# Kernel optimization log

Measured on AMD Instinct MI355X. Metric: run time of the kernel, lower is better.

The kernel has to match this reference:

```python
import jax, jax.numpy as jnp
import numpy as np

IMG = 64
NZ = 100
ENC_H = 800
DEC_H = 1600
IN_SZ = IMG * IMG  # 4096
D_ENC_IN = 2 * IN_SZ * 3 + DEC_H  # 26176


def setup_inputs() -> dict:
    key = jax.random.key(0)
    ks = jax.random.split(key, 12)
    B, T = 64, 10
    s = 0.02  # weight init scale to keep gates in sane range
    return {
        "x": jax.random.uniform(ks[0], (B, 3, IMG, IMG), jnp.float32),
        "noise": jax.random.normal(ks[1], (T, B, NZ), jnp.float32),
        "W_ih_mu": jax.random.normal(ks[2], (4 * ENC_H, D_ENC_IN), jnp.float32) * s,
        "W_hh_mu": jax.random.normal(ks[3], (4 * ENC_H, ENC_H), jnp.float32) * s,
        "b_mu": jnp.zeros((4 * ENC_H,), jnp.float32),
        "W_ih_lv": jax.random.normal(ks[4], (4 * ENC_H, D_ENC_IN), jnp.float32) * s,
        "W_hh_lv": jax.random.normal(ks[5], (4 * ENC_H, ENC_H), jnp.float32) * s,
        "b_lv": jnp.zeros((4 * ENC_H,), jnp.float32),
        "W_mu_fc": jax.random.normal(ks[6], (NZ, ENC_H), jnp.float32) * s,
        "b_mu_fc": jnp.zeros((NZ,), jnp.float32),
        "W_lv_fc": jax.random.normal(ks[7], (NZ, ENC_H), jnp.float32) * s,
        "b_lv_fc": jnp.zeros((NZ,), jnp.float32),
        "W_ih_dec": jax.random.normal(ks[8], (4 * DEC_H, NZ), jnp.float32) * s,
        "W_hh_dec": jax.random.normal(ks[9], (4 * DEC_H, DEC_H), jnp.float32) * s,
        "b_dec": jnp.zeros((4 * DEC_H,), jnp.float32),
        "W_write": jax.random.normal(ks[10], (3 * IN_SZ, DEC_H), jnp.float32) * s,
        "b_write": jnp.zeros((3 * IN_SZ,), jnp.float32),
        "T": T,
    }


def _lstm_cell(xin, h, c, W_ih, W_hh, b):
    # torch LSTMCell: gates ordered i, f, g, o
    g = xin @ W_ih.T + h @ W_hh.T + b
    i, f, gg, o = jnp.split(g, 4, axis=1)
    c_new = jax.nn.sigmoid(f) * c + jax.nn.sigmoid(i) * jnp.tanh(gg)
    h_new = jax.nn.sigmoid(o) * jnp.tanh(c_new)
    return h_new, c_new


def reference(x, noise, W_ih_mu, W_hh_mu, b_mu, W_ih_lv, W_hh_lv, b_lv,
              W_mu_fc, b_mu_fc, W_lv_fc, b_lv_fc,
              W_ih_dec, W_hh_dec, b_dec, W_write, b_write, T):
    B = x.shape[0]
    x_flat = x.reshape(B, -1)  # [B, 3*64*64]
    init = (
        jnp.zeros((B, 3, IMG, IMG), x.dtype),   # canvas c
        jnp.zeros((B, ENC_H), x.dtype), jnp.zeros((B, ENC_H), x.dtype),  # h_mu, c_mu
        jnp.zeros((B, ENC_H), x.dtype), jnp.zeros((B, ENC_H), x.dtype),  # h_lv, c_lv
        jnp.zeros((B, DEC_H), x.dtype), jnp.zeros((B, DEC_H), x.dtype),  # h_dec, c_dec
    )

    def step(carry, eps):
        c, h_mu, c_mu, h_lv, c_lv, h_dec, c_dec = carry
        sb = jax.nn.sigmoid(c)
        x_hat = (x - sb).reshape(B, -1)
        enc_in = jnp.concatenate([x_flat, x_hat, h_dec], axis=1)  # [B, 26176]
        h_mu, c_mu = _lstm_cell(enc_in, h_mu, c_mu, W_ih_mu, W_hh_mu, b_mu)
        mu = jax.nn.relu(h_mu @ W_mu_fc.T + b_mu_fc)
        h_lv, c_lv = _lstm_cell(enc_in, h_lv, c_lv, W_ih_lv, W_hh_lv, b_lv)
        logvar = jax.nn.relu(h_lv @ W_lv_fc.T + b_lv_fc)
        z = eps * jnp.exp(0.5 * logvar) + mu
        h_dec, c_dec = _lstm_cell(z, h_dec, c_dec, W_ih_dec, W_hh_dec, b_dec)
        wr = (h_dec @ W_write.T + b_write).reshape(B, 3, IMG, IMG)
        c = c + wr
        return (c, h_mu, c_mu, h_lv, c_lv, h_dec, c_dec), (mu, logvar)

    (c, *_), (mu_t, logvar_t) = jax.lax.scan(step, init, noise)
    return jax.nn.sigmoid(c), mu_t, logvar_t
```

## Files before the change

kernel.cpp:

```cpp
#include <hip/hip_runtime.h>

typedef __attribute__((ext_vector_type(8))) short bf16x8;
typedef __attribute__((ext_vector_type(4))) float f32x4;
typedef __attribute__((ext_vector_type(4))) int i32x4;
typedef unsigned int u32;

#define B_SZ   64
#define IMGSZ  12288
#define ENC_H  800
#define DEC_H  1600
#define NZ     100
#define NENC   6400
#define KHH    832
#define KDEC   1728
#define GSZ    (B_SZ*NENC)
#define SLICES 7
#define G0SL   8

#define WQMUL    1008.0f
#define SCALE_I8 (-1.0f/(254.0f*1008.0f))

__device__ __forceinline__ unsigned short f2bf(float f){
  unsigned u = __float_as_uint(f);
  u += 0x7fffu + ((u >> 16) & 1u);
  return (unsigned short)(u >> 16);
}
__device__ __forceinline__ float bf2f(unsigned short h){
  return __uint_as_float(((unsigned)h) << 16);
}
__device__ __forceinline__ float sigf(float x){ return 1.f/(1.f + __expf(-x)); }
__device__ __forceinline__ ushort4 cv4(float4 v){
  ushort4 o; o.x=f2bf(v.x); o.y=f2bf(v.y); o.z=f2bf(v.z); o.w=f2bf(v.w); return o;
}
__device__ __forceinline__ unsigned q4(float4 v){
  int a = __float2int_rn(fminf(fmaxf(v.x*WQMUL, -127.f), 127.f));
  int b = __float2int_rn(fminf(fmaxf(v.y*WQMUL, -127.f), 127.f));
  int c = __float2int_rn(fminf(fmaxf(v.z*WQMUL, -127.f), 127.f));
  int d = __float2int_rn(fminf(fmaxf(v.w*WQMUL, -127.f), 127.f));
  return (a&255) | ((b&255)<<8) | ((c&255)<<16) | ((d&255)<<24);
}

__device__ __forceinline__ void gllb(const void* g, void* l){
  __builtin_amdgcn_global_load_lds((const __attribute__((address_space(1))) u32*)g,
                                   (__attribute__((address_space(3))) u32*)l, 16, 0, 0);
}

__device__ __forceinline__ void gemm_lds3(const unsigned short* __restrict__ A, int lda, int k0,
                                          const unsigned short* __restrict__ Bpk, size_t bchunk0,
                                          int nchb, unsigned short (*sm)[4096], f32x4 acc[4])
{
  const int tid = threadIdx.x;
  const int lane = tid & 63, w = tid >> 6;
  const int l15 = lane & 15, lg = lane >> 4;
  const int l8 = lane >> 3, l7 = lane & 7;

  const unsigned short* gA0 = A + (size_t)(w*16 + l8)*lda + k0 + (l7 ^ l8)*8;
  const unsigned short* gA1 = gA0 + (size_t)8*lda;
  const unsigned short* gB0 = Bpk + bchunk0*4096 + w*1024 + lane*8;

#pragma unroll
  for (int m = 0; m < 4; ++m) acc[m] = (f32x4){0.f,0.f,0.f,0.f};

  gllb(gA0, &sm[0][(w*2+0)*512]);
  gllb(gA1, &sm[0][(w*2+1)*512]);
  gllb(gB0,       &sm[1][w*1024]);
  gllb(gB0 + 512, &sm[1][w*1024 + 512]);
  if (1 < nchb){
    gllb(gA0 + 64, &sm[2][(w*2+0)*512]);
    gllb(gA1 + 64, &sm[2][(w*2+1)*512]);
    gllb(gB0 + 4096,       &sm[3][w*1024]);
    gllb(gB0 + 4096 + 512, &sm[3][w*1024 + 512]);
  }

  int cur = 0, nxt = 2;
  for (int c = 0; c < nchb; ++c){
    if (c + 1 < nchb) { asm volatile("s_waitcnt vmcnt(4)" ::: "memory"); }
    else              { asm volatile("s_waitcnt vmcnt(0)" ::: "memory"); }
    asm volatile("s_barrier" ::: "memory");
    const unsigned short* sa = sm[cur*2];
    const unsigned short* sb = sm[cur*2 + 1];
#pragma unroll
    for (int h = 0; h < 2; ++h){
      const int su8 = ((h*4 + lg) ^ (l15 & 7)) * 8;
      bf16x8 bfr = *(const bf16x8*)&sb[(w*16 + l15)*64 + su8];
#pragma unroll
      for (int m = 0; m < 4; ++m){
        bf16x8 afr = *(const bf16x8*)&sa[(m*16 + l15)*64 + su8];
        acc[m] = __builtin_amdgcn_mfma_f32_16x16x32_bf16(afr, bfr, acc[m], 0,0,0);
      }
    }
    if (c + 2 < nchb){
      const size_t ao = (size_t)(c+2)*64, bo = (size_t)(c+2)*4096;
      gllb(gA0 + ao, &sm[nxt*2][(w*2+0)*512]);
      gllb(gA1 + ao, &sm[nxt*2][(w*2+1)*512]);
      gllb(gB0 + bo,       &sm[nxt*2+1][w*1024]);
      gllb(gB0 + bo + 512, &sm[nxt*2+1][w*1024 + 512]);
    }
    cur = (cur==2) ? 0 : cur+1;
    nxt = (nxt==2) ? 0 : nxt+1;
  }
}

__device__ __forceinline__ void gemm_i8(const signed char* __restrict__ A, int lda, int k0,
                                        const signed char* __restrict__ Bpk, size_t bch0,
                                        int nch, unsigned char* sm, i32x4 acc[4])
{
  const int tid = threadIdx.x;
  const int lane = tid & 63, w = tid >> 6;
  const int l15 = lane & 15, lg = lane >> 4;

  const int rp = lane >> 3, un = lane & 7;
  const int swz = un ^ (rp & 7);
  const int rloc = rp*2 + ((swz >> 2) & 1);
  const int uA = swz & 3;
  const signed char* gA = A + (size_t)(w*16 + rloc)*lda + k0 + uA*16;
  const signed char* gB = Bpk + bch0*4096 + w*1024 + lane*16;

#pragma unroll
  for (int m = 0; m < 4; ++m) acc[m] = (i32x4){0,0,0,0};

  {
    gllb(gA, sm + 0*8192 + w*1024 + lane*16);
    gllb(gB, sm + 0*8192 + 4096 + w*1024 + lane*16);
    if (1 < nch){
      gllb(gA + 64,   sm + 1*8192 + w*1024 + lane*16);
      gllb(gB + 4096, sm + 1*8192 + 4096 + w*1024 + lane*16);
    }
  }

  const int rB = w*16 + l15;
  const int offB = 4096 + (rB>>1)*128 + (((((rB&1)<<2) + lg) ^ ((rB>>1)&7))*16);

  int cur = 0, nxt = 2;
  for (int c = 0; c < nch; ++c){
    if (c + 1 < nch) { asm volatile("s_waitcnt vmcnt(2)" ::: "memory"); }
    else             { asm volatile("s_waitcnt vmcnt(0)" ::: "memory"); }
    asm volatile("s_barrier" ::: "memory");
    const unsigned char* s = sm + cur*8192;
    i32x4 bfr = *(const i32x4*)(s + offB);
#pragma unroll
    for (int m = 0; m < 4; ++m){
      int rA = m*16 + l15;
      i32x4 afr = *(const i32x4*)(s + (rA>>1)*128 + (((((rA&1)<<2) + lg) ^ ((rA>>1)&7))*16));
      acc[m] = __builtin_amdgcn_mfma_i32_16x16x64_i8(afr, bfr, acc[m], 0, 0, 0);
    }
    if (c + 2 < nch){
      gllb(gA + (size_t)(c+2)*64,   sm + nxt*8192 + w*1024 + lane*16);
      gllb(gB + (size_t)(c+2)*4096, sm + nxt*8192 + 4096 + w*1024 + lane*16);
    }
    cur = (cur==2) ? 0 : cur+1;
    nxt = (nxt==2) ? 0 : nxt+1;
  }
}

__device__ __forceinline__ void store_out1(f32x4 acc[4], float* __restrict__ Out,
                                           int ldo, int col0){
  const int lane = threadIdx.x & 63, w = threadIdx.x >> 6;
  const int l15 = lane & 15, lg = lane >> 4;
  int col = col0 + w*16 + l15;
#pragma unroll
  for (int m = 0; m < 4; ++m)
#pragma unroll
    for (int j = 0; j < 4; ++j)
      Out[(size_t)(m*16 + lg*4 + j)*ldo + col] = acc[m][j];
}

__device__ __forceinline__ void store_i8(i32x4 acc[4], float* __restrict__ Out,
                                         int ldo, int col0){
  const int lane = threadIdx.x & 63, w = threadIdx.x >> 6;
  const int l15 = lane & 15, lg = lane >> 4;
  int col = col0 + w*16 + l15;
#pragma unroll
  for (int m = 0; m < 4; ++m)
#pragma unroll
    for (int j = 0; j < 4; ++j)
      Out[(size_t)(m*16 + lg*4 + j)*ldo + col] = SCALE_I8 * (float)acc[m][j];
}

#define R_ENCM 19200
#define R_WHC  21700
#define R_WHH  23000
#define R_WDEC 25700
#define R_WWR  30500
#define R_MISC 31425
#define M_FC   40000u
#define M_XBF  236608u

__global__ __launch_bounds__(256) void k_pack_all(
    const float* __restrict__ Wihmu, const float* __restrict__ Wihlv,
    const float* __restrict__ Whhmu, const float* __restrict__ Whhlv,
    const float* __restrict__ Whhdec, const float* __restrict__ Wihdec,
    const float* __restrict__ Wwrite, const float* __restrict__ Wmufc,
    const float* __restrict__ Wlvfc, const float* __restrict__ x,
    unsigned short* __restrict__ wab, unsigned char* __restrict__ wi8,
    float* __restrict__ csPart, unsigned short* __restrict__ whc,
    unsigned short* __restrict__ whh, unsigned short* __restrict__ wdec,
    unsigned short* __restrict__ wwr, unsigned short* __restrict__ wfcmu,
    unsigned short* __restrict__ wfclv, unsigned short* __restrict__ xbf)
{
  int bid = blockIdx.x;
  if (bid < R_ENCM){
    __shared__ float cs[256];
    int ch = bid % 192, cb = bid / 192;
    int t = threadIdx.x;
    int r = t >> 2, seg = t & 3;
    int col = cb*64 + r;
    const float4* src = (col < 3200) ? ((const float4*)Wihmu + (size_t)col*6544)
                                     : ((const float4*)Wihlv + (size_t)(col-3200)*6544);
    int k4b = ch*16 + seg*4;
    float4 va[4], vb[4];
#pragma unroll
    for (int i = 0; i < 4; ++i){ va[i] = src[k4b+i]; vb[i] = src[3072 + k4b + i]; }

    ushort4* wabT = (ushort4*)wab + ((size_t)cb*192 + ch)*1024;
#pragma unroll
    for (int d = 0; d < 2; ++d){
      int u16 = seg*2 + d;
      int su = u16 ^ (r & 7);
      float4 s0, s1;
      s0.x=va[2*d].x+vb[2*d].x;   s0.y=va[2*d].y+vb[2*d].y;
      s0.z=va[2*d].z+vb[2*d].z;   s0.w=va[2*d].w+vb[2*d].w;
      s1.x=va[2*d+1].x+vb[2*d+1].x; s1.y=va[2*d+1].y+vb[2*d+1].y;
      s1.z=va[2*d+1].z+vb[2*d+1].z; s1.w=va[2*d+1].w+vb[2*d+1].w;
      wabT[r*16 + su*2 + 0] = cv4(s0);
      wabT[r*16 + su*2 + 1] = cv4(s1);
    }

    unsigned char* wi8T = wi8 + ((size_t)cb*192 + ch)*4096;
    int unit = (((r&1)<<2) + seg) ^ ((r>>1) & 7);
    uint4 pk;
    pk.x = q4(vb[0]); pk.y = q4(vb[1]); pk.z = q4(vb[2]); pk.w = q4(vb[3]);
    *(uint4*)(wi8T + (r>>1)*128 + unit*16) = pk;

    float s = 0.f;
#pragma unroll
    for (int i = 0; i < 4; ++i) s += vb[i].x + vb[i].y + vb[i].z + vb[i].w;
    cs[t] = s;
    __syncthreads();
    if (seg == 0)
      csPart[((size_t)col)*192 + ch] = cs[t] + cs[t+1] + cs[t+2] + cs[t+3];
  }
  else if (bid < R_WHC){
    int i = bid - R_ENCM;
    int ch = i % 25, cb = i / 25;
    ushort4* whcT = (ushort4*)whc + ((size_t)cb*25 + ch)*1024;
#pragma unroll
    for (int qv = 0; qv < 4; ++qv){
      int ou = qv*256 + threadIdx.x;
      int r = ou >> 4, qq = ou & 15;
      int su = qq >> 1, half = qq & 1;
      int uu = su ^ (r & 7);
      int k4 = ch*16 + uu*2 + half;
      int col = cb*64 + r;
      const float4* src = (col < 3200) ? ((const float4*)Wihmu + (size_t)col*6544)
                                       : ((const float4*)Wihlv + (size_t)(col-3200)*6544);
      whcT[ou] = cv4(src[6144 + k4]);
    }
  }
  else if (bid < R_WHH){
    int i = bid - R_WHC;
    int ch = i % 13, cb = i / 13;
    ushort4* whhT = (ushort4*)whh + ((size_t)cb*13 + ch)*1024;
#pragma unroll
    for (int qv = 0; qv < 4; ++qv){
      int ou = qv*256 + threadIdx.x;
      int r = ou >> 4, qq = ou & 15;
      int su = qq >> 1, half = qq & 1;
      int uu = su ^ (r & 7);
      int k4 = ch*16 + uu*2 + half;
      int col = cb*64 + r;
      float4 v = {0.f,0.f,0.f,0.f};
      if (k4 < 200)
        v = (col < 3200) ? ((const float4*)Whhmu)[(size_t)col*200 + k4]
                         : ((const float4*)Whhlv)[(size_t)(col-3200)*200 + k4];
      whhT[ou] = cv4(v);
    }
  }
  else if (bid < R_WDEC){
    int i = bid - R_WHH;
    int ch = i % 27, cb = i / 27;
    ushort4* wdecT = (ushort4*)wdec + ((size_t)cb*27 + ch)*1024;
#pragma unroll
    for (int qv = 0; qv < 4; ++qv){
      int ou = qv*256 + threadIdx.x;
      int r = ou >> 4, qq = ou & 15;
      int su = qq >> 1, half = qq & 1;
      int uu = su ^ (r & 7);
      int k4 = ch*16 + uu*2 + half;
      int pr = cb*64 + r;
      unsigned j = pr >> 2, g = pr & 3, srow = g*1600u + j;
      float4 v = {0.f,0.f,0.f,0.f};
      if (k4 < 400)      v = ((const float4*)Whhdec)[(size_t)srow*400 + k4];
      else if (k4 < 425) v = ((const float4*)Wihdec)[(size_t)srow*25 + (k4-400)];
      wdecT[ou] = cv4(v);
    }
  }
  else if (bid < R_WWR){
    int i = bid - R_WDEC;
    int ch = i % 25, cb = i / 25;
    ushort4* wwrT = (ushort4*)wwr + ((size_t)cb*25 + ch)*1024;
#pragma unroll
    for (int qv = 0; qv < 4; ++qv){
      int ou = qv*256 + threadIdx.x;
      int r = ou >> 4, qq = ou & 15;
      int su = qq >> 1, half = qq & 1;
      int uu = su ^ (r & 7);
      int k4 = ch*16 + uu*2 + half;
      int p = cb*64 + r;
      wwrT[ou] = cv4(((const float4*)Wwrite)[(size_t)p*400 + k4]);
    }
  }
  else {
    unsigned i = (unsigned)(bid - R_WWR)*256u + threadIdx.x;
    if (i >= M_XBF) return;
    if (i < M_FC){
      if (i < 20000u) ((ushort4*)wfcmu)[i] = cv4(((const float4*)Wmufc)[i]);
      else            ((ushort4*)wfclv)[i-20000u] = cv4(((const float4*)Wlvfc)[i-20000u]);
    } else {
      unsigned j = i - M_FC;
      ((ushort4*)xbf)[j] = cv4(((const float4*)x)[j]);
    }
  }
}

__global__ __launch_bounds__(256) void k_csred(const float* __restrict__ csPart,
                                               float* __restrict__ colsum){
  unsigned col = blockIdx.x*blockDim.x + threadIdx.x;
  if (col >= NENC) return;
  const float* p = csPart + (size_t)col*192;
  float s = 0.f;
#pragma unroll 8
  for (int ch = 0; ch < 192; ++ch) s += p[ch];
  colsum[col] = s;
}


__global__ __launch_bounds__(256) void k_g0(const unsigned short* __restrict__ xbf,
                                            const unsigned short* __restrict__ wab,
                                            float* __restrict__ gpart){
  __shared__ __align__(16) unsigned short smem[6][4096];
  int bid = blockIdx.x;
  int s = bid/100, cb = bid - s*100;
  f32x4 acc[4];
  gemm_lds3(xbf, IMGSZ, s*1536, wab, (size_t)cb*192 + s*24, 24, smem, acc);
  store_out1(acc, gpart + (size_t)s*GSZ, NENC, cb*64);
}

__global__ __launch_bounds__(256) void k_g0red(const float* __restrict__ gpart,
                                               float* __restrict__ g0){
  unsigned i = blockIdx.x*blockDim.x + threadIdx.x;
  if (i >= GSZ) return;
  float s = 0.f;
#pragma unroll
  for (int p = 0; p < G0SL; ++p) s += gpart[(size_t)p*GSZ + i];
  g0[i] = s;
}

__global__ __launch_bounds__(256) void k_enc(const signed char* __restrict__ ui8,
                                             const signed char* __restrict__ wi8,
                                             const unsigned short* __restrict__ uhd,
                                             const unsigned short* __restrict__ whc,
                                             const unsigned short* __restrict__ hmup,
                                             const unsigned short* __restrict__ hlvp,
                                             const unsigned short* __restrict__ whh,
                                             float* __restrict__ gpart){
  __shared__ __align__(16) unsigned char smem[49152];
  int bid = blockIdx.x;
  if (bid < 500){
    int s = bid/100, cb = bid - s*100;
    int ch0 = s*38 + (s < 2 ? s : 2);
    int nch = 38 + (s < 2 ? 1 : 0);
    i32x4 acc[4];
    gemm_i8(ui8, IMGSZ, ch0*64, wi8, (size_t)cb*192 + ch0, nch, smem, acc);
    store_i8(acc, gpart + (size_t)s*GSZ, NENC, cb*64);
  } else if (bid < 600){
    int cb = bid - 500;
    f32x4 acc[4];
    gemm_lds3(uhd, DEC_H, 0, whc, (size_t)cb*25, 25,
              (unsigned short (*)[4096])smem, acc);
    store_out1(acc, gpart + (size_t)5*GSZ, NENC, cb*64);
  } else {
    int cb = bid - 600;
    const unsigned short* A = (cb < 50) ? hmup : hlvp;
    f32x4 acc[4];
    gemm_lds3(A, KHH, 0, whh, (size_t)cb*13, 13,
              (unsigned short (*)[4096])smem, acc);
    store_out1(acc, gpart + (size_t)6*GSZ, NENC, cb*64);
  }
}

__global__ __launch_bounds__(512) void k_cell(const float* __restrict__ g0,
                                              const float* __restrict__ gpart,
                                              const float* __restrict__ colsum,
                                              const float* __restrict__ bmu,
                                              const float* __restrict__ blv,
                                              float* __restrict__ cmu,
                                              float* __restrict__ clv,
                                              unsigned short* __restrict__ hmup,
                                              unsigned short* __restrict__ hlvp,
                                              const unsigned short* __restrict__ wfcmu,
                                              const unsigned short* __restrict__ wfclv,
                                              const float* __restrict__ bmufc,
                                              const float* __restrict__ blvfc,
                                              const float* __restrict__ noise_t,
                                              float* __restrict__ outMu,
                                              float* __restrict__ outLv,
                                              unsigned short* __restrict__ u2z){
  __shared__ float hsh[1600];
  __shared__ float red[512];
  int b = blockIdx.x, tid = threadIdx.x;

  for (int uidx = tid; uidx < 1600; uidx += 512){
    int which = uidx >= 800;
    int j = uidx - which*800;
    const float* bias = which ? blv : bmu;
    int cbase = which*3200 + j;
    size_t rowoff = (size_t)b*NENC + cbase;
    float a0 = bias[j]       - 0.5f*colsum[cbase];
    float a1 = bias[800+j]   - 0.5f*colsum[cbase+800];
    float a2 = bias[1600+j]  - 0.5f*colsum[cbase+1600];
    float a3 = bias[2400+j]  - 0.5f*colsum[cbase+2400];
    const float* q = g0 + rowoff;
    a0 += q[0]; a1 += q[800]; a2 += q[1600]; a3 += q[2400];
#pragma unroll
    for (int s = 0; s < SLICES; ++s){
      const float* p = gpart + (size_t)s*GSZ + rowoff;
      a0 += p[0]; a1 += p[800]; a2 += p[1600]; a3 += p[2400];
    }
    float* C = which ? clv : cmu;
    float cold = C[(size_t)b*ENC_H + j];
    float cn = sigf(a1)*cold + sigf(a0)*tanhf(a2);
    float h  = sigf(a3)*tanhf(cn);
    C[(size_t)b*ENC_H + j] = cn;
    (which ? hlvp : hmup)[(size_t)b*KHH + j] = f2bf(h);
    hsh[uidx] = h;
  }
  __syncthreads();

  if (tid < 400){
    int o = tid >> 1, half = tid & 1;
    int ismu = o < 100;
    int row = ismu ? o : o - 100;
    const unsigned short* wrow = (ismu ? wfcmu : wfclv) + (size_t)row*ENC_H + half*400;
    const float* hbase = hsh + (ismu ? 0 : 800) + half*400;
    float s = 0.f;
#pragma unroll 4
    for (int k = 0; k < 100; ++k){
      ushort4 wv = ((const ushort4*)wrow)[k];
      s += bf2f(wv.x)*hbase[k*4]   + bf2f(wv.y)*hbase[k*4+1]
         + bf2f(wv.z)*hbase[k*4+2] + bf2f(wv.w)*hbase[k*4+3];
    }
    red[tid] = s;
  }
  __syncthreads();
  if (tid < 200){
    int o = tid; int ismu = o < 100; int row = ismu ? o : o - 100;
    float s = red[2*o] + red[2*o+1] + (ismu ? bmufc[row] : blvfc[row]);
    s = fmaxf(s, 0.f);
    if (ismu) outMu[(size_t)b*NZ + row] = s;
    else      outLv[(size_t)b*NZ + row] = s;
    hsh[o] = s;
  }
  __syncthreads();
  if (tid < 100){
    float mu = hsh[tid], lv = hsh[100 + tid];
    float z = noise_t[(size_t)b*NZ + tid]*__expf(0.5f*lv) + mu;
    u2z[(size_t)b*KDEC + DEC_H + tid] = f2bf(z);
  }
}

__global__ __launch_bounds__(256) void k_dec(const unsigned short* __restrict__ u2r,
                                             const unsigned short* __restrict__ wdec,
                                             const float* __restrict__ bdec,
                                             float* __restrict__ cdec,
                                             unsigned short* __restrict__ uhd,
                                             unsigned short* __restrict__ u2w){
  __shared__ __align__(16) unsigned short smem[6][4096];
  int bid = blockIdx.x;
  f32x4 acc[4];
  gemm_lds3(u2r, KDEC, 0, wdec, (size_t)bid*27, 27, smem, acc);
  __syncthreads();
  float* lds = (float*)&smem[0][0];
  const int lane = threadIdx.x & 63;
  const int wave = threadIdx.x >> 6;
  const int l15 = lane & 15, lg = lane >> 4;
#pragma unroll
  for (int m = 0; m < 4; ++m)
#pragma unroll
    for (int j = 0; j < 4; ++j)
      lds[(m*16 + lg*4 + j)*65 + wave*16 + l15] = acc[m][j];
  __syncthreads();
#pragma unroll
  for (int p = 0; p < 4; ++p){
    int idx = threadIdx.x + p*256;
    int b = idx & 63, jj = idx >> 6;
    const float* g4 = &lds[b*65 + jj*4];
    int j = bid*16 + jj;
    float gi = g4[0] + bdec[j];
    float gf = g4[1] + bdec[DEC_H + j];
    float gg = g4[2] + bdec[2*DEC_H + j];
    float go = g4[3] + bdec[3*DEC_H + j];
    float cold = cdec[(size_t)b*DEC_H + j];
    float cn = sigf(gf)*cold + sigf(gi)*tanhf(gg);
    float h  = sigf(go)*tanhf(cn);
    cdec[(size_t)b*DEC_H + j] = cn;
    unsigned short hb = f2bf(h);
    u2w[(size_t)b*KDEC + j] = hb;
    uhd[(size_t)b*DEC_H + j] = hb;
  }
}

__global__ __launch_bounds__(256) void k_write(const unsigned short* __restrict__ u2,
                                               const unsigned short* __restrict__ wwr,
                                               const float* __restrict__ bwr,
                                               float* __restrict__ canvas,
                                               signed char* __restrict__ ui8){
  __shared__ __align__(16) unsigned short smem[6][4096];
  f32x4 acc[4];
  gemm_lds3(u2, KDEC, 0, wwr, (size_t)blockIdx.x*25, 25, smem, acc);
  const int lane = threadIdx.x & 63;
  const int wave = threadIdx.x >> 6;
  const int l15 = lane & 15, lg = lane >> 4;
  int col = blockIdx.x*64 + wave*16 + l15;
#pragma unroll
  for (int m = 0; m < 4; ++m){
#pragma unroll
    for (int j = 0; j < 4; ++j){
      int row = m*16 + lg*4 + j;
      float cv = canvas[(size_t)row*IMGSZ + col] + acc[m][j] + bwr[col];
      canvas[(size_t)row*IMGSZ + col] = cv;
      ui8[(size_t)row*IMGSZ + col] =
        (signed char)__float2int_rn((sigf(cv) - 0.5f)*254.f);
    }
  }
}

__global__ __launch_bounds__(256) void k_final(const float* __restrict__ canvas,
                                               float* __restrict__ out){
  unsigned i = blockIdx.x*blockDim.x + threadIdx.x;
  if (i < (unsigned)(B_SZ*IMGSZ)) out[i] = sigf(canvas[i]);
}

constexpr size_t SZ_WAB    = (size_t)NENC*IMGSZ*2;
constexpr size_t SZ_WI8    = (size_t)NENC*IMGSZ;
constexpr size_t SZ_WHC    = (size_t)NENC*DEC_H*2;
constexpr size_t SZ_WHH    = (size_t)NENC*KHH*2;
constexpr size_t SZ_WDEC   = (size_t)NENC*KDEC*2;
constexpr size_t SZ_WWR    = (size_t)IMGSZ*DEC_H*2;
constexpr size_t SZ_WFC    = (size_t)NZ*ENC_H*2;
constexpr size_t SZ_XBF    = (size_t)B_SZ*IMGSZ*2;
constexpr size_t SZ_CSPART = (size_t)NENC*192*4;
constexpr size_t SZ_CSUM   = (size_t)NENC*4;
constexpr size_t SZ_G0     = (size_t)GSZ*4;
constexpr size_t SZ_GPART  = (size_t)G0SL*GSZ*4;
constexpr size_t SZ_CANVAS = (size_t)B_SZ*IMGSZ*4;
constexpr size_t SZ_CMU    = (size_t)B_SZ*ENC_H*4;
constexpr size_t SZ_CDEC   = (size_t)B_SZ*DEC_H*4;
constexpr size_t SZ_HP     = (size_t)B_SZ*KHH*2;
constexpr size_t SZ_UHD    = (size_t)B_SZ*DEC_H*2;
constexpr size_t SZ_U2     = (size_t)B_SZ*KDEC*2;
constexpr size_t SZ_UI8    = (size_t)B_SZ*IMGSZ;

constexpr size_t OFF_WAB    = 0;
constexpr size_t OFF_WI8    = OFF_WAB    + SZ_WAB;
constexpr size_t OFF_WHC    = OFF_WI8    + SZ_WI8;
constexpr size_t OFF_WHH    = OFF_WHC    + SZ_WHC;
constexpr size_t OFF_WDEC   = OFF_WHH    + SZ_WHH;
constexpr size_t OFF_WWR    = OFF_WDEC   + SZ_WDEC;
constexpr size_t OFF_WFCMU  = OFF_WWR    + SZ_WWR;
constexpr size_t OFF_WFCLV  = OFF_WFCMU  + SZ_WFC;
constexpr size_t OFF_XBF    = OFF_WFCLV  + SZ_WFC;
constexpr size_t OFF_CSPART = OFF_XBF    + SZ_XBF;
constexpr size_t OFF_CSUM   = OFF_CSPART + SZ_CSPART;
constexpr size_t OFF_G0     = OFF_CSUM   + SZ_CSUM;
constexpr size_t OFF_GPART  = OFF_G0     + SZ_G0;
constexpr size_t OFF_CANVAS = OFF_GPART  + SZ_GPART;
constexpr size_t OFF_CMU    = OFF_CANVAS + SZ_CANVAS;
constexpr size_t OFF_CLV    = OFF_CMU    + SZ_CMU;
constexpr size_t OFF_CDEC   = OFF_CLV    + SZ_CMU;
constexpr size_t OFF_HMUP   = OFF_CDEC   + SZ_CDEC;
constexpr size_t OFF_HLVP   = OFF_HMUP   + SZ_HP;
constexpr size_t OFF_UHD    = OFF_HLVP   + SZ_HP;
constexpr size_t OFF_U2A    = OFF_UHD    + SZ_UHD;
constexpr size_t OFF_U2B    = OFF_U2A    + SZ_U2;
constexpr size_t OFF_UI8    = OFF_U2B    + SZ_U2;
constexpr size_t OFF_END    = OFF_UI8    + SZ_UI8;

extern "C" void kernel_launch(void* const* d_in, const int* in_sizes, int n_in,
                              void* d_out, int out_size, void* d_ws, size_t ws_size,
                              hipStream_t stream) {
  const float* x      = (const float*)d_in[0];
  const float* noise  = (const float*)d_in[1];
  const float* Wihmu  = (const float*)d_in[2];
  const float* Whhmu  = (const float*)d_in[3];
  const float* bmu    = (const float*)d_in[4];
  const float* Wihlv  = (const float*)d_in[5];
  const float* Whhlv  = (const float*)d_in[6];
  const float* blv    = (const float*)d_in[7];
  const float* Wmufc  = (const float*)d_in[8];
  const float* bmufc  = (const float*)d_in[9];
  const float* Wlvfc  = (const float*)d_in[10];
  const float* blvfc  = (const float*)d_in[11];
  const float* Wihdec = (const float*)d_in[12];
  const float* Whhdec = (const float*)d_in[13];
  const float* bdec   = (const float*)d_in[14];
  const float* Wwrite = (const float*)d_in[15];
  const float* bwrite = (const float*)d_in[16];
  int T = in_sizes[1] / (B_SZ*NZ);

  if (ws_size < OFF_END) return;

  char* ws = (char*)d_ws;
  unsigned short* wab   = (unsigned short*)(ws + OFF_WAB);
  unsigned char*  wi8   = (unsigned char*)(ws + OFF_WI8);
  unsigned short* whc   = (unsigned short*)(ws + OFF_WHC);
  unsigned short* whh   = (unsigned short*)(ws + OFF_WHH);
  unsigned short* wdec  = (unsigned short*)(ws + OFF_WDEC);
  unsigned short* wwr   = (unsigned short*)(ws + OFF_WWR);
  unsigned short* wfcmu = (unsigned short*)(ws + OFF_WFCMU);
  unsigned short* wfclv = (unsigned short*)(ws + OFF_WFCLV);
  unsigned short* xbf   = (unsigned short*)(ws + OFF_XBF);
  float* csPart = (float*)(ws + OFF_CSPART);
  float* colsum = (float*)(ws + OFF_CSUM);
  float* g0     = (float*)(ws + OFF_G0);
  float* gpart  = (float*)(ws + OFF_GPART);
  float* canvas = (float*)(ws + OFF_CANVAS);
  float* cmu    = (float*)(ws + OFF_CMU);
  float* clv    = (float*)(ws + OFF_CLV);
  float* cdec   = (float*)(ws + OFF_CDEC);
  unsigned short* hmup = (unsigned short*)(ws + OFF_HMUP);
  unsigned short* hlvp = (unsigned short*)(ws + OFF_HLVP);
  unsigned short* uhd  = (unsigned short*)(ws + OFF_UHD);
  unsigned short* u2[2] = { (unsigned short*)(ws + OFF_U2A),
                            (unsigned short*)(ws + OFF_U2B) };
  signed char* ui8 = (signed char*)(ws + OFF_UI8);

  float* out = (float*)d_out;
  float* outMu = out + (size_t)B_SZ*IMGSZ;
  float* outLv = outMu + (size_t)T*B_SZ*NZ;

  dim3 blk(256);

  k_pack_all<<<R_MISC, blk, 0, stream>>>(Wihmu, Wihlv, Whhmu, Whhlv,
                                         Whhdec, Wihdec, Wwrite, Wmufc, Wlvfc, x,
                                         wab, wi8, csPart, whc, whh, wdec, wwr,
                                         wfcmu, wfclv, xbf);
  k_csred<<<(NENC + 255)/256, blk, 0, stream>>>(csPart, colsum);
  hipMemsetAsync(ws + OFF_CANVAS, 0, OFF_END - OFF_CANVAS, stream);

  k_g0<<<800, blk, 0, stream>>>(xbf, wab, gpart);
  k_g0red<<<GSZ/256, blk, 0, stream>>>(gpart, g0);

  for (int t = 0; t < T; ++t){
    unsigned short* u2r = u2[t & 1];
    unsigned short* u2w = u2[(t + 1) & 1];
    k_enc<<<700, blk, 0, stream>>>(ui8, (const signed char*)wi8, uhd, whc,
                                   hmup, hlvp, whh, gpart);
    k_cell<<<B_SZ, 512, 0, stream>>>(g0, gpart, colsum, bmu, blv, cmu, clv,
                                     hmup, hlvp, wfcmu, wfclv, bmufc, blvfc,
                                     noise + (size_t)t*B_SZ*NZ,
                                     outMu + (size_t)t*B_SZ*NZ,
                                     outLv + (size_t)t*B_SZ*NZ, u2r);
    k_dec<<<100, blk, 0, stream>>>(u2r, wdec, bdec, cdec, uhd, u2w);
    k_write<<<IMGSZ/64, blk, 0, stream>>>(u2w, wwr, bwrite, canvas, ui8);
  }

  k_final<<<(B_SZ*IMGSZ)/256, blk, 0, stream>>>(canvas, out);
}
```

Before: 929.3 us.

## Hoist decoder recurrent GEMM into encoder kernel, shrink dependent decoder kernel

The decoder's h_dec@W_hh part no longer depends on z, so it now runs as extra blocks inside k_enc, overlapping with the encoder GEMMs and writing to a new gdecH buffer. k_decz then only does the small z GEMM (2 K-chunks) plus the gate epilogue, which shortens the serial critical path through k_cell→k_dec. The int8 image GEMM is also re-split from 5 slices of about 38 chunks to 3 slices of 64, which cuts the number of partial sums k_cell has to reduce but makes each block longer. The extra gdecH buffer costs one more fp32 round-trip per step.

```diff
diff --git a/kernel.cpp b/kernel.cpp
--- a/kernel.cpp
+++ b/kernel.cpp
@@ -14,7 +14,7 @@
 #define KHH    832
 #define KDEC   1728
 #define GSZ    (B_SZ*NENC)
-#define SLICES 7
+#define SLICES 5
 #define G0SL   8
 
 #define WQMUL    1008.0f
@@ -363,29 +363,36 @@
                                              const unsigned short* __restrict__ hmup,
                                              const unsigned short* __restrict__ hlvp,
                                              const unsigned short* __restrict__ whh,
-                                             float* __restrict__ gpart){
+                                             const unsigned short* __restrict__ wdec,
+                                             float* __restrict__ gpart,
+                                             float* __restrict__ gdecH){
   __shared__ __align__(16) unsigned char smem[49152];
   int bid = blockIdx.x;
-  if (bid < 500){
+  if (bid < 300){
     int s = bid/100, cb = bid - s*100;
-    int ch0 = s*38 + (s < 2 ? s : 2);
-    int nch = 38 + (s < 2 ? 1 : 0);
+    int ch0 = s*64;
     i32x4 acc[4];
-    gemm_i8(ui8, IMGSZ, ch0*64, wi8, (size_t)cb*192 + ch0, nch, smem, acc);
+    gemm_i8(ui8, IMGSZ, ch0*64, wi8, (size_t)cb*192 + ch0, 64, smem, acc);
     store_i8(acc, gpart + (size_t)s*GSZ, NENC, cb*64);
-  } else if (bid < 600){
-    int cb = bid - 500;
+  } else if (bid < 400){
+    int cb = bid - 300;
     f32x4 acc[4];
     gemm_lds3(uhd, DEC_H, 0, whc, (size_t)cb*25, 25,
               (unsigned short (*)[4096])smem, acc);
-    store_out1(acc, gpart + (size_t)5*GSZ, NENC, cb*64);
-  } else {
-    int cb = bid - 600;
+    store_out1(acc, gpart + (size_t)3*GSZ, NENC, cb*64);
+  } else if (bid < 500){
+    int cb = bid - 400;
     const unsigned short* A = (cb < 50) ? hmup : hlvp;
     f32x4 acc[4];
     gemm_lds3(A, KHH, 0, whh, (size_t)cb*13, 13,
               (unsigned short (*)[4096])smem, acc);
-    store_out1(acc, gpart + (size_t)6*GSZ, NENC, cb*64);
+    store_out1(acc, gpart + (size_t)4*GSZ, NENC, cb*64);
+  } else {
+    int cb = bid - 500;
+    f32x4 acc[4];
+    gemm_lds3(uhd, DEC_H, 0, wdec, (size_t)cb*27, 25,
+              (unsigned short (*)[4096])smem, acc);
+    store_out1(acc, gdecH, NENC, cb*64);
   }
 }
 
@@ -405,7 +412,7 @@
                                               const float* __restrict__ noise_t,
                                               float* __restrict__ outMu,
                                               float* __restrict__ outLv,
-                                              unsigned short* __restrict__ u2z){
+                                              unsigned short* __restrict__ uz){
   __shared__ float hsh[1600];
   __shared__ float red[512];
   int b = blockIdx.x, tid = threadIdx.x;
@@ -465,25 +472,33 @@
   if (tid < 100){
     float mu = hsh[tid], lv = hsh[100 + tid];
     float z = noise_t[(size_t)b*NZ + tid]*__expf(0.5f*lv) + mu;
-    u2z[(size_t)b*KDEC + DEC_H + tid] = f2bf(z);
-  }
-}
-
-__global__ __launch_bounds__(256) void k_dec(const unsigned short* __restrict__ u2r,
-                                             const unsigned short* __restrict__ wdec,
-                                             const float* __restrict__ bdec,
-                                             float* __restrict__ cdec,
-                                             unsigned short* __restrict__ uhd,
-                                             unsigned short* __restrict__ u2w){
+    uz[(size_t)b*128 + tid] = f2bf(z);
+  }
+}
+
+__global__ __launch_bounds__(256) void k_decz(const unsigned short* __restrict__ uz,
+                                              const unsigned short* __restrict__ wdec,
+                                              const float* __restrict__ gdecH,
+                                              const float* __restrict__ bdec,
+                                              float* __restrict__ cdec,
+                                              unsigned short* __restrict__ uhd){
   __shared__ __align__(16) unsigned short smem[6][4096];
   int bid = blockIdx.x;
   f32x4 acc[4];
-  gemm_lds3(u2r, KDEC, 0, wdec, (size_t)bid*27, 27, smem, acc);
-  __syncthreads();
-  float* lds = (float*)&smem[0][0];
+  gemm_lds3(uz, 128, 0, wdec, (size_t)bid*27 + 25, 2, smem, acc);
   const int lane = threadIdx.x & 63;
   const int wave = threadIdx.x >> 6;
   const int l15 = lane & 15, lg = lane >> 4;
+  {
+    int col = bid*64 + wave*16 + l15;
+#pragma unroll
+    for (int m = 0; m < 4; ++m)
+#pragma unroll
+      for (int j = 0; j < 4; ++j)
+        acc[m][j] += gdecH[(size_t)(m*16 + lg*4 + j)*NENC + col];
+  }
+  __syncthreads();
+  float* lds = (float*)&smem[0][0];
 #pragma unroll
   for (int m = 0; m < 4; ++m)
 #pragma unroll
@@ -504,20 +519,18 @@
     float cn = sigf(gf)*cold + sigf(gi)*tanhf(gg);
     float h  = sigf(go)*tanhf(cn);
     cdec[(size_t)b*DEC_H + j] = cn;
-    unsigned short hb = f2bf(h);
-    u2w[(size_t)b*KDEC + j] = hb;
-    uhd[(size_t)b*DEC_H + j] = hb;
-  }
-}
-
-__global__ __launch_bounds__(256) void k_write(const unsigned short* __restrict__ u2,
+    uhd[(size_t)b*DEC_H + j] = f2bf(h);
+  }
+}
+
+__global__ __launch_bounds__(256) void k_write(const unsigned short* __restrict__ uhd,
                                                const unsigned short* __restrict__ wwr,
                                                const float* __restrict__ bwr,
                                                float* __restrict__ canvas,
                                                signed char* __restrict__ ui8){
   __shared__ __align__(16) unsigned short smem[6][4096];
   f32x4 acc[4];
-  gemm_lds3(u2, KDEC, 0, wwr, (size_t)blockIdx.x*25, 25, smem, acc);
+  gemm_lds3(uhd, DEC_H, 0, wwr, (size_t)blockIdx.x*25, 25, smem, acc);
   const int lane = threadIdx.x & 63;
   const int wave = threadIdx.x >> 6;
   const int l15 = lane & 15, lg = lane >> 4;
@@ -553,12 +566,13 @@
 constexpr size_t SZ_CSUM   = (size_t)NENC*4;
 constexpr size_t SZ_G0     = (size_t)GSZ*4;
 constexpr size_t SZ_GPART  = (size_t)G0SL*GSZ*4;
+constexpr size_t SZ_GDECH  = (size_t)B_SZ*NENC*4;
 constexpr size_t SZ_CANVAS = (size_t)B_SZ*IMGSZ*4;
 constexpr size_t SZ_CMU    = (size_t)B_SZ*ENC_H*4;
 constexpr size_t SZ_CDEC   = (size_t)B_SZ*DEC_H*4;
 constexpr size_t SZ_HP     = (size_t)B_SZ*KHH*2;
 constexpr size_t SZ_UHD    = (size_t)B_SZ*DEC_H*2;
-constexpr size_t SZ_U2     = (size_t)B_SZ*KDEC*2;
+constexpr size_t SZ_UZ     = (size_t)B_SZ*128*2;
 constexpr size_t SZ_UI8    = (size_t)B_SZ*IMGSZ;
 
 constexpr size_t OFF_WAB    = 0;
@@ -574,16 +588,16 @@
 constexpr size_t OFF_CSUM   = OFF_CSPART + SZ_CSPART;
 constexpr size_t OFF_G0     = OFF_CSUM   + SZ_CSUM;
 constexpr size_t OFF_GPART  = OFF_G0     + SZ_G0;
-constexpr size_t OFF_CANVAS = OFF_GPART  + SZ_GPART;
+constexpr size_t OFF_GDECH  = OFF_GPART  + SZ_GPART;
+constexpr size_t OFF_CANVAS = OFF_GDECH  + SZ_GDECH;
 constexpr size_t OFF_CMU    = OFF_CANVAS + SZ_CANVAS;
 constexpr size_t OFF_CLV    = OFF_CMU    + SZ_CMU;
 constexpr size_t OFF_CDEC   = OFF_CLV    + SZ_CMU;
 constexpr size_t OFF_HMUP   = OFF_CDEC   + SZ_CDEC;
 constexpr size_t OFF_HLVP   = OFF_HMUP   + SZ_HP;
 constexpr size_t OFF_UHD    = OFF_HLVP   + SZ_HP;
-constexpr size_t OFF_U2A    = OFF_UHD    + SZ_UHD;
-constexpr size_t OFF_U2B    = OFF_U2A    + SZ_U2;
-constexpr size_t OFF_UI8    = OFF_U2B    + SZ_U2;
+constexpr size_t OFF_UZ     = OFF_UHD    + SZ_UHD;
+constexpr size_t OFF_UI8    = OFF_UZ     + SZ_UZ;
 constexpr size_t OFF_END    = OFF_UI8    + SZ_UI8;
 
 extern "C" void kernel_launch(void* const* d_in, const int* in_sizes, int n_in,
@@ -624,6 +638,7 @@
   float* colsum = (float*)(ws + OFF_CSUM);
   float* g0     = (float*)(ws + OFF_G0);
   float* gpart  = (float*)(ws + OFF_GPART);
+  float* gdecH  = (float*)(ws + OFF_GDECH);
   float* canvas = (float*)(ws + OFF_CANVAS);
   float* cmu    = (float*)(ws + OFF_CMU);
   float* clv    = (float*)(ws + OFF_CLV);
@@ -631,8 +646,7 @@
   unsigned short* hmup = (unsigned short*)(ws + OFF_HMUP);
   unsigned short* hlvp = (unsigned short*)(ws + OFF_HLVP);
   unsigned short* uhd  = (unsigned short*)(ws + OFF_UHD);
-  unsigned short* u2[2] = { (unsigned short*)(ws + OFF_U2A),
-                            (unsigned short*)(ws + OFF_U2B) };
+  unsigned short* uz   = (unsigned short*)(ws + OFF_UZ);
   signed char* ui8 = (signed char*)(ws + OFF_UI8);
 
   float* out = (float*)d_out;
@@ -652,17 +666,15 @@
   k_g0red<<<GSZ/256, blk, 0, stream>>>(gpart, g0);
 
   for (int t = 0; t < T; ++t){
-    unsigned short* u2r = u2[t & 1];
-    unsigned short* u2w = u2[(t + 1) & 1];
-    k_enc<<<700, blk, 0, stream>>>(ui8, (const signed char*)wi8, uhd, whc,
-                                   hmup, hlvp, whh, gpart);
+    k_enc<<<600, blk, 0, stream>>>(ui8, (const signed char*)wi8, uhd, whc,
+                                   hmup, hlvp, whh, wdec, gpart, gdecH);
     k_cell<<<B_SZ, 512, 0, stream>>>(g0, gpart, colsum, bmu, blv, cmu, clv,
                                      hmup, hlvp, wfcmu, wfclv, bmufc, blvfc,
                                      noise + (size_t)t*B_SZ*NZ,
                                      outMu + (size_t)t*B_SZ*NZ,
-                                     outLv + (size_t)t*B_SZ*NZ, u2r);
-    k_dec<<<100, blk, 0, stream>>>(u2r, wdec, bdec, cdec, uhd, u2w);
-    k_write<<<IMGSZ/64, blk, 0, stream>>>(u2w, wwr, bwrite, canvas, ui8);
+                                     outLv + (size_t)t*B_SZ*NZ, uz);
+    k_decz<<<100, blk, 0, stream>>>(uz, wdec, gdecH, bdec, cdec, uhd);
+    k_write<<<IMGSZ/64, blk, 0, stream>>>(uhd, wwr, bwrite, canvas, ui8);
   }
 
   k_final<<<(B_SZ*IMGSZ)/256, blk, 0, stream>>>(canvas, out);
```

Result: faster. 904.4 us, median of 2 (-2.7%).
